# Performance work log

Measured on AMD Instinct MI355X. Metric: run time of the kernel, lower is better.

The kernel has to match this reference:

```python
import jax, jax.numpy as jnp
import numpy as np

N = 50000      # nodes
E = 1600000    # edges (avg degree 32)
D = 64         # d_node
DE = 32        # d_edge
H = 4          # heads
L = 3          # layers


def _ln(x, g, b):
    mu = x.mean(-1, keepdims=True)
    var = ((x - mu) ** 2).mean(-1, keepdims=True)
    return (x - mu) / jnp.sqrt(var + 1e-5) * g + b


def setup_inputs() -> dict:
    key = jax.random.key(0)
    ks = jax.random.split(key, 16)
    s = 0.05
    return {
        "node_features": jax.random.normal(ks[0], (N, D), jnp.float32),
        "edge_features": jax.random.normal(ks[1], (E, DE), jnp.float32),
        "edge_index": jax.random.randint(ks[2], (2, E), 0, N),
        "Wq": jax.random.normal(ks[3], (L, D, D), jnp.float32) * s,
        "Wk": jax.random.normal(ks[4], (L, D, D), jnp.float32) * s,
        "Wv": jax.random.normal(ks[5], (L, D, D), jnp.float32) * s,
        "Wo": jax.random.normal(ks[6], (L, D, D), jnp.float32) * s,
        "We": jax.random.normal(ks[7], (L, DE, H), jnp.float32) * s,   # edge-conditioned score bias
        "Wem": jax.random.normal(ks[8], (L, 2 * D + DE, DE), jnp.float32) * s,
        "bem": jnp.zeros((L, DE), jnp.float32),
        "gn": jnp.ones((L, D), jnp.float32),
        "bn": jnp.zeros((L, D), jnp.float32),
        "ge": jnp.ones((L, DE), jnp.float32),
        "be": jnp.zeros((L, DE), jnp.float32),
    }


def _delta_forward(h, e, src, dst, Wq, Wk, Wv, Wo, We, Wem, bem, gn, bn, ge, be):
    n = h.shape[0]
    dh = D // H
    for i in range(L):
        # --- node attention over edges (sparse, per-dst segment softmax) ---
        q = (h @ Wq[i]).reshape(n, H, dh)
        k = (h @ Wk[i]).reshape(n, H, dh)
        v = (h @ Wv[i]).reshape(n, H, dh)
        scores = jnp.einsum('ehd,ehd->eh', q[dst], k[src]) / jnp.sqrt(jnp.float32(dh))
        scores = scores + e @ We[i]                         # edge-conditioned bias [E,H]
        m = jax.ops.segment_max(scores, dst, num_segments=n)
        p = jnp.exp(scores - m[dst])
        denom = jax.ops.segment_sum(p, dst, num_segments=n)
        alpha = p / (denom[dst] + 1e-9)                      # [E,H]
        msg = (alpha[:, :, None] * v[src]).reshape(-1, D)    # [E,D]
        agg = jax.ops.segment_sum(msg, dst, num_segments=n)  # [N,D]
        h = _ln(h + agg @ Wo[i], gn[i], bn[i])
        # --- edge update conditioned on endpoint nodes ---
        emsg = jax.nn.gelu(jnp.concatenate([h[src], h[dst], e], axis=-1) @ Wem[i] + bem[i])
        e = _ln(e + emsg, ge[i], be[i])
    return h


def reference(node_features, edge_features, edge_index, Wq, Wk, Wv, Wo, We, Wem, bem, gn, bn, ge, be):
    src = edge_index[0]
    dst = edge_index[1]
    return _delta_forward(node_features, edge_features, src, dst,
                          Wq, Wk, Wv, Wo, We, Wem, bem, gn, bn, ge, be)
```

## Files before the change

### kernel.cpp

```cpp
#include <hip/hip_runtime.h>
#include <hip/hip_bf16.h>
#include <math.h>

#define NN 50000
#define NE 1600000
#define D 64
#define DE 32
#define H 4
#define DH 16
#define L 3

typedef __attribute__((ext_vector_type(8))) short bf16x8;
typedef __attribute__((ext_vector_type(8))) short s16x8;
typedef __attribute__((ext_vector_type(4))) float f32x4;

__device__ __forceinline__ short f2b(float f) {
    __hip_bfloat16 h = __float2bfloat16(f);
    short s;
    __builtin_memcpy(&s, &h, 2);
    return s;
}
__device__ __forceinline__ float b2f(unsigned short u) {
    unsigned int x = ((unsigned int)u) << 16;
    float f; __builtin_memcpy(&f, &x, 4); return f;
}
__device__ __forceinline__ float b2f_lo(unsigned int p) {
    unsigned int x = p << 16;
    float f; __builtin_memcpy(&f, &x, 4); return f;
}
__device__ __forceinline__ float b2f_hi(unsigned int p) {
    unsigned int x = p & 0xffff0000u;
    float f; __builtin_memcpy(&f, &x, 4); return f;
}


__global__ void deg_kernel(const int* __restrict__ dst, int* __restrict__ cnt) {
    int e = blockIdx.x * 256 + threadIdx.x;
    if (e >= NE) return;
    atomicAdd(&cnt[dst[e]], 1);
}

__global__ void block_sum_kernel(const int* __restrict__ cnt, int* __restrict__ bsum) {
    int b = blockIdx.x, t = threadIdx.x;
    int base = b * 1024 + t * 4;
    int s = 0;
#pragma unroll
    for (int i = 0; i < 4; i++) { int idx = base + i; if (idx < NN) s += cnt[idx]; }
#pragma unroll
    for (int off = 32; off; off >>= 1) s += __shfl_down(s, off);
    __shared__ int wsum[4];
    if ((t & 63) == 0) wsum[t >> 6] = s;
    __syncthreads();
    if (t == 0) bsum[b] = wsum[0] + wsum[1] + wsum[2] + wsum[3];
}

__global__ void scan_bsum_kernel(int* __restrict__ bsum, int nb) {
    if (blockIdx.x == 0 && threadIdx.x == 0) {
        int run = 0;
        for (int i = 0; i < nb; i++) { int c = bsum[i]; bsum[i] = run; run += c; }
    }
}

__global__ void scan_block_kernel(const int* __restrict__ cnt, const int* __restrict__ bsum,
                                  int* __restrict__ offsets) {
    int b = blockIdx.x, t = threadIdx.x;
    int base = b * 1024 + t * 4;
    int v[4]; int s = 0;
#pragma unroll
    for (int i = 0; i < 4; i++) { int idx = base + i; v[i] = (idx < NN) ? cnt[idx] : 0; s += v[i]; }
    int lane = t & 63, w = t >> 6;
    int x = s;
#pragma unroll
    for (int off = 1; off < 64; off <<= 1) {
        int y = __shfl_up(x, off);
        if (lane >= off) x += y;
    }
    __shared__ int wsum[4];
    if (lane == 63) wsum[w] = x;
    __syncthreads();
    int woff = 0;
    for (int i = 0; i < w; i++) woff += wsum[i];
    int run = bsum[b] + woff + x - s;
#pragma unroll
    for (int i = 0; i < 4; i++) {
        int idx = base + i;
        if (idx < NN) offsets[idx] = run;
        run += v[i];
    }
}

__global__ void scatter_kernel(const int* __restrict__ src, const int* __restrict__ dst,
                               const int* __restrict__ offsets,
                               int* __restrict__ cursor,
                               int* __restrict__ sorted_eid,
                               int* __restrict__ sorted_src,
                               int* __restrict__ sorted_dst) {
    int e = blockIdx.x * 256 + threadIdx.x;
    if (e >= NE) return;
    int d0 = dst[e];
    int pos = atomicAdd(&cursor[d0], 1);
    int position = offsets[d0] + pos;
    sorted_eid[position] = e;
    sorted_src[position] = src[e];
    sorted_dst[position] = d0;
}

__global__ void eperm_kernel(const float* __restrict__ e32, const int* __restrict__ sorted_eid,
                             const float* __restrict__ We0,
                             unsigned short* __restrict__ eb_s,
                             float* __restrict__ ebias_s) {
    int t = blockIdx.x * 256 + threadIdx.x;
    if (t >= NE * 4) return;
    int p = t >> 2;
    int c = (t & 3) * 8;
    int eid = sorted_eid[p];
    const float* ep = e32 + (size_t)eid * DE + c;
    float4 x0 = *(const float4*)(ep);
    float4 x1 = *(const float4*)(ep + 4);
    float e8[8] = {x0.x, x0.y, x0.z, x0.w, x1.x, x1.y, x1.z, x1.w};
    s16x8 ob;
#pragma unroll
    for (int i = 0; i < 8; i++) ob[i] = f2b(e8[i]);
    *(s16x8*)(eb_s + (size_t)p * DE + c) = ob;
    float p0 = 0.f, p1 = 0.f, p2 = 0.f, p3 = 0.f;
#pragma unroll
    for (int i = 0; i < 8; i++) {
        float4 w = *(const float4*)(We0 + (c + i) * 4);
        p0 += e8[i] * w.x; p1 += e8[i] * w.y; p2 += e8[i] * w.z; p3 += e8[i] * w.w;
    }
#pragma unroll
    for (int off = 1; off < 4; off <<= 1) {
        p0 += __shfl_xor(p0, off, 4);
        p1 += __shfl_xor(p1, off, 4);
        p2 += __shfl_xor(p2, off, 4);
        p3 += __shfl_xor(p3, off, 4);
    }
    if ((t & 3) == 0) {
        float4 o; o.x = p0; o.y = p1; o.z = p2; o.w = p3;
        *(float4*)(ebias_s + (size_t)p * H) = o;
    }
}

__global__ void wconv_kernel(const float* __restrict__ Wem, unsigned short* __restrict__ Wt) {
    int t = blockIdx.x * 256 + threadIdx.x;
    if (t >= L * 32 * 160) return;
    int l = t / 5120;
    int r = t % 5120;
    int n = r / 160;
    int k = r % 160;
    Wt[t] = (unsigned short)f2b(Wem[l * 5120 + k * 32 + n]);
}

__global__ void wsplit_kernel(const float* __restrict__ Wq, const float* __restrict__ Wk,
                              const float* __restrict__ Wv, const float* __restrict__ Wo,
                              unsigned short* __restrict__ WT_hi,
                              unsigned short* __restrict__ WT_lo) {
    int t = blockIdx.x * 256 + threadIdx.x;
    if (t >= L * 4 * 64 * 64) return;
    int k = t & 63;
    int n = (t >> 6) & 63;
    int mat = (t >> 12) & 3;
    int l = t >> 14;
    const float* W = (mat == 0) ? Wq : (mat == 1) ? Wk : (mat == 2) ? Wv : Wo;
    float w = W[l * 4096 + k * 64 + n];
    unsigned short hi = (unsigned short)f2b(w);
    float lo = w - b2f(hi);
    WT_hi[t] = hi;
    WT_lo[t] = (unsigned short)f2b(lo);
}

__global__ void hconv_kernel(const float* __restrict__ nf, float* __restrict__ h,
                             unsigned short* __restrict__ hb) {
    int t = blockIdx.x * 256 + threadIdx.x;
    if (t >= NN * D) return;
    float x = nf[t];
    h[t] = x;
    hb[t] = (unsigned short)f2b(x);
}


__global__ __launch_bounds__(256, 8)
void qkv_kernel(const float* __restrict__ h,
                const unsigned short* __restrict__ WT_hi,
                const unsigned short* __restrict__ WT_lo,
                float* __restrict__ q, unsigned int* __restrict__ kv) {
    int lane = threadIdx.x & 63;
    int wv = threadIdx.x >> 6;
    int m = lane & 15, quad = lane >> 4;
    int base = blockIdx.x * 16;

    const float* hp = h + (size_t)(base + m) * D + quad * 8;
    float af[16];
    *(f32x4*)&af[0]  = *(const f32x4*)(hp);
    *(f32x4*)&af[4]  = *(const f32x4*)(hp + 4);
    *(f32x4*)&af[8]  = *(const f32x4*)(hp + 32);
    *(f32x4*)&af[12] = *(const f32x4*)(hp + 36);
    bf16x8 a0h, a0l, a1h, a1l;
#pragma unroll
    for (int j = 0; j < 8; j++) {
        short h0 = f2b(af[j]);
        short h1 = f2b(af[8 + j]);
        a0h[j] = h0; a0l[j] = f2b(af[j] - b2f((unsigned short)h0));
        a1h[j] = h1; a1l[j] = f2b(af[8 + j] - b2f((unsigned short)h1));
    }

    f32x4 acc[3];
#pragma unroll
    for (int mat = 0; mat < 3; mat++) {
        const unsigned short* bh = WT_hi + ((size_t)mat * 64 + wv * 16 + m) * 64 + quad * 8;
        const unsigned short* bl = WT_lo + ((size_t)mat * 64 + wv * 16 + m) * 64 + quad * 8;
        bf16x8 bh0 = *(const bf16x8*)(bh);
        bf16x8 bh1 = *(const bf16x8*)(bh + 32);
        bf16x8 bl0 = *(const bf16x8*)(bl);
        bf16x8 bl1 = *(const bf16x8*)(bl + 32);
        f32x4 c = {0.f, 0.f, 0.f, 0.f};
        c = __builtin_amdgcn_mfma_f32_16x16x32_bf16(a0h, bh0, c, 0, 0, 0);
        c = __builtin_amdgcn_mfma_f32_16x16x32_bf16(a1h, bh1, c, 0, 0, 0);
        c = __builtin_amdgcn_mfma_f32_16x16x32_bf16(a0h, bl0, c, 0, 0, 0);
        c = __builtin_amdgcn_mfma_f32_16x16x32_bf16(a1h, bl1, c, 0, 0, 0);
        c = __builtin_amdgcn_mfma_f32_16x16x32_bf16(a0l, bh0, c, 0, 0, 0);
        c = __builtin_amdgcn_mfma_f32_16x16x32_bf16(a1l, bh1, c, 0, 0, 0);
        acc[mat] = c;
    }

#pragma unroll
    for (int reg = 0; reg < 4; reg++) {
        int row = base + quad * 4 + reg;
        int col = wv * 16 + m;
        q[(size_t)row * D + col] = acc[0][reg] * 0.25f;
        unsigned int kb = (unsigned short)f2b(acc[1][reg]);
        unsigned int vb = (unsigned short)f2b(acc[2][reg]);
        kv[(size_t)row * D + col] = (vb << 16) | kb;
    }
}

__global__ void attn_kernel(const float* __restrict__ q, const unsigned int* __restrict__ kv,
                            const float* __restrict__ ebias_s,
                            const int* __restrict__ sorted_src,
                            const int* __restrict__ offsets,
                            float* __restrict__ agg) {
    int node = blockIdx.x * 4 + threadIdx.y;
    node = __builtin_amdgcn_readfirstlane(node);
    if (node >= NN) return;
    int lane = threadIdx.x;
    int hh = lane >> 4;
    float qv = q[node * D + lane];
    int beg = offsets[node];
    int end = (node == NN - 1) ? NE : offsets[node + 1];
    float mmax = -INFINITY, den = 0.f, acc = 0.f;
    int i = beg;
    for (; i + 8 <= end; i += 8) {
        int ss[8]; unsigned int kk8[8]; float bb8[8], dd[8];
#pragma unroll
        for (int u = 0; u < 8; u++) ss[u] = sorted_src[i + u];
#pragma unroll
        for (int u = 0; u < 8; u++) kk8[u] = kv[ss[u] * D + lane];
#pragma unroll
        for (int u = 0; u < 8; u++) bb8[u] = ebias_s[(i + u) * H + hh];
#pragma unroll
        for (int u = 0; u < 8; u++) dd[u] = qv * b2f_lo(kk8[u]);
#pragma unroll
        for (int off = 1; off < 16; off <<= 1) {
#pragma unroll
            for (int u = 0; u < 8; u++) dd[u] += __shfl_xor(dd[u], off, 16);
        }
        float nm = mmax;
#pragma unroll
        for (int u = 0; u < 8; u++) { dd[u] += bb8[u]; nm = fmaxf(nm, dd[u]); }
        float scale = __expf(mmax - nm);
        float ps = 0.f, av = 0.f;
#pragma unroll
        for (int u = 0; u < 8; u++) {
            float p = __expf(dd[u] - nm);
            ps += p;
            av += p * b2f_hi(kk8[u]);
        }
        den = den * scale + ps;
        acc = acc * scale + av;
        mmax = nm;
    }
    for (; i < end; i++) {
        int s = sorted_src[i];
        unsigned int kvv = kv[s * D + lane];
        float b = ebias_s[i * H + hh];
        float dot = qv * b2f_lo(kvv);
#pragma unroll
        for (int off = 1; off < 16; off <<= 1) dot += __shfl_xor(dot, off, 16);
        float score = dot + b;
        float nm = fmaxf(mmax, score);
        float scale = __expf(mmax - nm);
        float p = __expf(score - nm);
        den = den * scale + p;
        acc = acc * scale + p * b2f_hi(kvv);
        mmax = nm;
    }
    agg[node * D + lane] = acc / (den + 1e-9f);
}

__global__ __launch_bounds__(256, 8)
void node_update_kernel(float* __restrict__ h, const float* __restrict__ agg,
                        const unsigned short* __restrict__ WoT_hi,
                        const unsigned short* __restrict__ WoT_lo,
                        const float* __restrict__ gn,
                        const float* __restrict__ bn,
                        unsigned short* __restrict__ hb) {
    __shared__ float sx[16][68];
    int lane = threadIdx.x & 63;
    int wv = threadIdx.x >> 6;
    int m = lane & 15, quad = lane >> 4;
    int base = blockIdx.x * 16;

    const float* ap = agg + (size_t)(base + m) * D + quad * 8;
    float af[16];
    *(f32x4*)&af[0]  = *(const f32x4*)(ap);
    *(f32x4*)&af[4]  = *(const f32x4*)(ap + 4);
    *(f32x4*)&af[8]  = *(const f32x4*)(ap + 32);
    *(f32x4*)&af[12] = *(const f32x4*)(ap + 36);
    bf16x8 a0h, a0l, a1h, a1l;
#pragma unroll
    for (int j = 0; j < 8; j++) {
        short h0 = f2b(af[j]);
        short h1 = f2b(af[8 + j]);
        a0h[j] = h0; a0l[j] = f2b(af[j] - b2f((unsigned short)h0));
        a1h[j] = h1; a1l[j] = f2b(af[8 + j] - b2f((unsigned short)h1));
    }
    const unsigned short* bh = WoT_hi + ((size_t)wv * 16 + m) * 64 + quad * 8;
    const unsigned short* bl = WoT_lo + ((size_t)wv * 16 + m) * 64 + quad * 8;
    bf16x8 bh0 = *(const bf16x8*)(bh);
    bf16x8 bh1 = *(const bf16x8*)(bh + 32);
    bf16x8 bl0 = *(const bf16x8*)(bl);
    bf16x8 bl1 = *(const bf16x8*)(bl + 32);
    f32x4 c = {0.f, 0.f, 0.f, 0.f};
    c = __builtin_amdgcn_mfma_f32_16x16x32_bf16(a0h, bh0, c, 0, 0, 0);
    c = __builtin_amdgcn_mfma_f32_16x16x32_bf16(a1h, bh1, c, 0, 0, 0);
    c = __builtin_amdgcn_mfma_f32_16x16x32_bf16(a0h, bl0, c, 0, 0, 0);
    c = __builtin_amdgcn_mfma_f32_16x16x32_bf16(a1h, bl1, c, 0, 0, 0);
    c = __builtin_amdgcn_mfma_f32_16x16x32_bf16(a0l, bh0, c, 0, 0, 0);
    c = __builtin_amdgcn_mfma_f32_16x16x32_bf16(a1l, bh1, c, 0, 0, 0);

#pragma unroll
    for (int reg = 0; reg < 4; reg++) {
        int row = quad * 4 + reg;
        int col = wv * 16 + m;
        sx[row][col] = c[reg] + h[(size_t)(base + row) * D + col];
    }
    __syncthreads();

    float gcol = gn[lane], bcol = bn[lane];
#pragma unroll
    for (int it = 0; it < 4; it++) {
        int ln = wv * 4 + it;
        int node = base + ln;
        float x = sx[ln][lane];
        float sum = x, sq = x * x;
#pragma unroll
        for (int off = 32; off; off >>= 1) {
            sum += __shfl_xor(sum, off);
            sq += __shfl_xor(sq, off);
        }
        float mu = sum * (1.f / 64.f);
        float var = sq * (1.f / 64.f) - mu * mu;
        float out = (x - mu) * rsqrtf(var + 1e-5f) * gcol + bcol;
        h[(size_t)node * D + lane] = out;
        hb[(size_t)node * D + lane] = (unsigned short)f2b(out);
    }
}

__global__ __launch_bounds__(256, 4)
void edge_update_mfma_kernel(const unsigned short* __restrict__ hb,
                             unsigned short* __restrict__ eb_s,
                             const int* __restrict__ sorted_src,
                             const int* __restrict__ sorted_dst,
                             const unsigned short* __restrict__ Wt,
                             const float* __restrict__ bem,
                             const float* __restrict__ ge,
                             const float* __restrict__ be,
                             const float* __restrict__ We_next,
                             float* __restrict__ ebias_s,
                             int do_bias, int do_estore) {
    __shared__ __align__(16) unsigned short sWt[32][168];
    __shared__ __align__(16) float ytr[4][16][36];
    int tid = threadIdx.x;
    int wave = tid >> 6;
    int lane = tid & 63;
    int we = blockIdx.x * 64 + wave * 16;
    int m = lane & 15;
    int quad = lane >> 4;
    int p_m = we + m;
    int s_idx = sorted_src[p_m], d_idx = sorted_dst[p_m];

    const unsigned short* as = hb + (size_t)s_idx * D + quad * 8;
    const unsigned short* ad = hb + (size_t)d_idx * D + quad * 8;
    bf16x8 a_s0 = *(const bf16x8*)(as);
    bf16x8 a_s1 = *(const bf16x8*)(as + 32);
    bf16x8 a_d0 = *(const bf16x8*)(ad);
    bf16x8 a_d1 = *(const bf16x8*)(ad + 32);
    bf16x8 ea = *(const bf16x8*)(eb_s + (size_t)p_m * DE + quad * 8);

    {
        const unsigned int* Wt32 = (const unsigned int*)Wt;
#pragma unroll
        for (int it = 0; it < 10; it++) {
            int i = tid + it * 256;
            int sh = i * 2;
            int r = sh / 160, c = sh % 160;
            *(unsigned int*)&sWt[r][c] = Wt32[i];
        }
    }

    bf16x8 wb;
#pragma unroll
    for (int j = 0; j < 8; j++) {
        float w = (do_bias && m < 4) ? We_next[(quad * 8 + j) * 4 + m] : 0.f;
        wb[j] = f2b(w);
    }

    __syncthreads();

    f32x4 c0 = {0.f, 0.f, 0.f, 0.f};
    f32x4 c1 = {0.f, 0.f, 0.f, 0.f};
    const unsigned short* w0 = &sWt[m][quad * 8];
    const unsigned short* w1 = &sWt[m + 16][quad * 8];

#pragma unroll
    for (int ks = 0; ks < 4; ks++) {
        bf16x8 a = (ks == 0) ? a_s0 : (ks == 1) ? a_s1 : (ks == 2) ? a_d0 : a_d1;
        bf16x8 b0 = *(const bf16x8*)(w0 + ks * 32);
        bf16x8 b1 = *(const bf16x8*)(w1 + ks * 32);
        c0 = __builtin_amdgcn_mfma_f32_16x16x32_bf16(a, b0, c0, 0, 0, 0);
        c1 = __builtin_amdgcn_mfma_f32_16x16x32_bf16(a, b1, c1, 0, 0, 0);
    }
    {
        bf16x8 b0 = *(const bf16x8*)(w0 + 4 * 32);
        bf16x8 b1 = *(const bf16x8*)(w1 + 4 * 32);
        c0 = __builtin_amdgcn_mfma_f32_16x16x32_bf16(ea, b0, c0, 0, 0, 0);
        c1 = __builtin_amdgcn_mfma_f32_16x16x32_bf16(ea, b1, c1, 0, 0, 0);
    }

    float bm0 = bem[m], bm1 = bem[m + 16];
#pragma unroll
    for (int reg = 0; reg < 4; reg++) {
        int row = quad * 4 + reg;
        float y0 = c0[reg] + bm0;
        float y1 = c1[reg] + bm1;
        float u0 = 1.5957691216057308f * (y0 + 0.044715f * y0 * y0 * y0);
        float u1 = 1.5957691216057308f * (y1 + 0.044715f * y1 * y1 * y1);
        float t0 = 1.f - 2.f / (1.f + __expf(u0));
        float t1 = 1.f - 2.f / (1.f + __expf(u1));
        ytr[wave][row][m] = 0.5f * y0 * (1.f + t0);
        ytr[wave][row][m + 16] = 0.5f * y1 * (1.f + t1);
    }
    __syncthreads();

    float y[8];
    *(f32x4*)&y[0] = *(const f32x4*)&ytr[wave][m][quad * 8];
    *(f32x4*)&y[4] = *(const f32x4*)&ytr[wave][m][quad * 8 + 4];
    float s = 0.f, sq = 0.f;
#pragma unroll
    for (int j = 0; j < 8; j++) {
        y[j] += b2f((unsigned short)ea[j]);
        s += y[j];
        sq += y[j] * y[j];
    }
    s += __shfl_xor(s, 16); s += __shfl_xor(s, 32);
    sq += __shfl_xor(sq, 16); sq += __shfl_xor(sq, 32);
    float mu = s * (1.f / 32.f);
    float var = sq * (1.f / 32.f) - mu * mu;
    float inv = rsqrtf(var + 1e-5f);

    float4 g0 = *(const float4*)(ge + quad * 8);
    float4 g1 = *(const float4*)(ge + quad * 8 + 4);
    float4 b0 = *(const float4*)(be + quad * 8);
    float4 b1 = *(const float4*)(be + quad * 8 + 4);
    float gg[8] = {g0.x, g0.y, g0.z, g0.w, g1.x, g1.y, g1.z, g1.w};
    float bbv[8] = {b0.x, b0.y, b0.z, b0.w, b1.x, b1.y, b1.z, b1.w};
    bf16x8 zb;
#pragma unroll
    for (int j = 0; j < 8; j++) {
        float z = (y[j] - mu) * inv * gg[j] + bbv[j];
        zb[j] = f2b(z);
    }
    if (do_estore) {
        *(s16x8*)(eb_s + (size_t)p_m * DE + quad * 8) = zb;
    }
    if (do_bias) {
        f32x4 db = {0.f, 0.f, 0.f, 0.f};
        db = __builtin_amdgcn_mfma_f32_16x16x32_bf16(zb, wb, db, 0, 0, 0);
        if (m < 4) {
#pragma unroll
            for (int reg = 0; reg < 4; reg++) {
                ebias_s[(we + quad * 4 + reg) * H + m] = db[reg];
            }
        }
    }
}

extern "C" void kernel_launch(void* const* d_in, const int* in_sizes, int n_in,
                              void* d_out, int out_size, void* d_ws, size_t ws_size,
                              hipStream_t stream) {
    const float* node_features = (const float*)d_in[0];
    const float* e = (const float*)d_in[1];
    const int* edge_index = (const int*)d_in[2];
    const int* src = edge_index;
    const int* dst = edge_index + NE;
    const float* Wq = (const float*)d_in[3];
    const float* Wk = (const float*)d_in[4];
    const float* Wv = (const float*)d_in[5];
    const float* Wo = (const float*)d_in[6];
    const float* We = (const float*)d_in[7];
    const float* Wem = (const float*)d_in[8];
    const float* bem = (const float*)d_in[9];
    const float* gn = (const float*)d_in[10];
    const float* bn = (const float*)d_in[11];
    const float* ge = (const float*)d_in[12];
    const float* be = (const float*)d_in[13];

    float* h = (float*)d_out;

    float* ws = (float*)d_ws;
    float* q = ws;
    unsigned int* kv = (unsigned int*)(q + NN * D);
    float* agg = (float*)(kv + NN * D);
    float* ebias_s = agg + NN * D;
    int* offsets = (int*)(ebias_s + (size_t)NE * H);
    int* cursor = offsets + NN;
    int* bsum = cursor + NN;
    int* sorted_eid = bsum + 64;
    int* sorted_src = sorted_eid + NE;
    int* sorted_dst = sorted_src + NE;
    unsigned short* Wt = (unsigned short*)(sorted_dst + NE);
    unsigned short* hb = Wt + L * 32 * 160;
    unsigned short* eb_s = hb + NN * D;
    unsigned short* WT_hi = eb_s + (size_t)NE * DE;
    unsigned short* WT_lo = WT_hi + L * 4 * 64 * 64;

    const int NB = (NN + 1023) / 1024;

    hipMemsetAsync(cursor, 0, NN * sizeof(int), stream);
    deg_kernel<<<(NE + 255) / 256, 256, 0, stream>>>(dst, cursor);
    block_sum_kernel<<<NB, 256, 0, stream>>>(cursor, bsum);
    scan_bsum_kernel<<<1, 64, 0, stream>>>(bsum, NB);
    scan_block_kernel<<<NB, 256, 0, stream>>>(cursor, bsum, offsets);
    hipMemsetAsync(cursor, 0, NN * sizeof(int), stream);
    scatter_kernel<<<(NE + 255) / 256, 256, 0, stream>>>(src, dst, offsets, cursor,
                                                         sorted_eid, sorted_src, sorted_dst);
    eperm_kernel<<<(NE * 4 + 255) / 256, 256, 0, stream>>>(e, sorted_eid, We, eb_s, ebias_s);
    wconv_kernel<<<(L * 32 * 160 + 255) / 256, 256, 0, stream>>>(Wem, Wt);
    wsplit_kernel<<<(L * 4 * 64 * 64 + 255) / 256, 256, 0, stream>>>(Wq, Wk, Wv, Wo,
                                                                     WT_hi, WT_lo);
    hconv_kernel<<<(NN * D + 255) / 256, 256, 0, stream>>>(node_features, h, hb);

    for (int layer = 0; layer < L; layer++) {
        const unsigned short* WT_hi_l = WT_hi + (size_t)layer * 4 * 4096;
        const unsigned short* WT_lo_l = WT_lo + (size_t)layer * 4 * 4096;
        const unsigned short* Wt_l = Wt + layer * 32 * 160;
        const float* bem_l = bem + layer * DE;
        const float* gn_l = gn + layer * D;
        const float* bn_l = bn + layer * D;
        const float* ge_l = ge + layer * DE;
        const float* be_l = be + layer * DE;

        qkv_kernel<<<NN / 16, 256, 0, stream>>>(h, WT_hi_l, WT_lo_l, q, kv);
        attn_kernel<<<NN / 4, dim3(64, 4), 0, stream>>>(q, kv, ebias_s, sorted_src,
                                                        offsets, agg);
        node_update_kernel<<<NN / 16, 256, 0, stream>>>(h, agg,
                                                        WT_hi_l + 3 * 4096,
                                                        WT_lo_l + 3 * 4096,
                                                        gn_l, bn_l, hb);
        if (layer < L - 1) {
            const float* We_next = We + (layer + 1) * DE * H;
            edge_update_mfma_kernel<<<NE / 64, 256, 0, stream>>>(hb, eb_s, sorted_src,
                                                                 sorted_dst, Wt_l,
                                                                 bem_l, ge_l, be_l,
                                                                 We_next, ebias_s,
                                                                 1, layer == 0 ? 1 : 0);
        }
    }
}
```

Before: 1.132 ms.

## Keep edge-update weights in registers and process four edge tiles per wave

The edge-update kernel no longer stages the 32x160 weight matrix in shared memory for every 64-edge block. Each wave now loads its weight fragments into registers once and loops over four 16-edge tiles, so there are four times fewer blocks and the block-wide barrier and shared-memory weight copy are gone. The sorted src/dst gather moves from the atomic scatter kernel into the coalesced eperm pass, and the single-thread serial block-sum scan becomes a wave shuffle scan. The cost is more registers per thread, which may lower occupancy, and less latency hiding within each wave because the gathers for each tile are done serially.

```diff
diff --git a/kernel.cpp b/kernel.cpp
--- a/kernel.cpp
+++ b/kernel.cpp
@@ -55,10 +55,15 @@
 }
 
 __global__ void scan_bsum_kernel(int* __restrict__ bsum, int nb) {
-    if (blockIdx.x == 0 && threadIdx.x == 0) {
-        int run = 0;
-        for (int i = 0; i < nb; i++) { int c = bsum[i]; bsum[i] = run; run += c; }
-    }
+    int t = threadIdx.x;
+    int v = (t < nb) ? bsum[t] : 0;
+    int x = v;
+#pragma unroll
+    for (int off = 1; off < 64; off <<= 1) {
+        int y = __shfl_up(x, off);
+        if (t >= off) x += y;
+    }
+    if (t < nb) bsum[t] = x - v;
 }
 
 __global__ void scan_block_kernel(const int* __restrict__ cnt, const int* __restrict__ bsum,
@@ -89,26 +94,24 @@
     }
 }
 
-__global__ void scatter_kernel(const int* __restrict__ src, const int* __restrict__ dst,
+__global__ void scatter_kernel(const int* __restrict__ dst,
                                const int* __restrict__ offsets,
                                int* __restrict__ cursor,
-                               int* __restrict__ sorted_eid,
-                               int* __restrict__ sorted_src,
-                               int* __restrict__ sorted_dst) {
+                               int* __restrict__ sorted_eid) {
     int e = blockIdx.x * 256 + threadIdx.x;
     if (e >= NE) return;
     int d0 = dst[e];
     int pos = atomicAdd(&cursor[d0], 1);
-    int position = offsets[d0] + pos;
-    sorted_eid[position] = e;
-    sorted_src[position] = src[e];
-    sorted_dst[position] = d0;
+    sorted_eid[offsets[d0] + pos] = e;
 }
 
 __global__ void eperm_kernel(const float* __restrict__ e32, const int* __restrict__ sorted_eid,
+                             const int* __restrict__ src, const int* __restrict__ dst,
                              const float* __restrict__ We0,
                              unsigned short* __restrict__ eb_s,
-                             float* __restrict__ ebias_s) {
+                             float* __restrict__ ebias_s,
+                             int* __restrict__ sorted_src,
+                             int* __restrict__ sorted_dst) {
     int t = blockIdx.x * 256 + threadIdx.x;
     if (t >= NE * 4) return;
     int p = t >> 2;
@@ -138,6 +141,8 @@
     if ((t & 3) == 0) {
         float4 o; o.x = p0; o.y = p1; o.z = p2; o.w = p3;
         *(float4*)(ebias_s + (size_t)p * H) = o;
+        sorted_src[p] = src[eid];
+        sorted_dst[p] = dst[eid];
     }
 }
 
@@ -378,118 +383,105 @@
                              const float* __restrict__ We_next,
                              float* __restrict__ ebias_s,
                              int do_bias, int do_estore) {
-    __shared__ __align__(16) unsigned short sWt[32][168];
     __shared__ __align__(16) float ytr[4][16][36];
     int tid = threadIdx.x;
     int wave = tid >> 6;
     int lane = tid & 63;
-    int we = blockIdx.x * 64 + wave * 16;
+    int wbase = blockIdx.x * 256 + wave * 64;
     int m = lane & 15;
     int quad = lane >> 4;
-    int p_m = we + m;
-    int s_idx = sorted_src[p_m], d_idx = sorted_dst[p_m];
-
-    const unsigned short* as = hb + (size_t)s_idx * D + quad * 8;
-    const unsigned short* ad = hb + (size_t)d_idx * D + quad * 8;
-    bf16x8 a_s0 = *(const bf16x8*)(as);
-    bf16x8 a_s1 = *(const bf16x8*)(as + 32);
-    bf16x8 a_d0 = *(const bf16x8*)(ad);
-    bf16x8 a_d1 = *(const bf16x8*)(ad + 32);
-    bf16x8 ea = *(const bf16x8*)(eb_s + (size_t)p_m * DE + quad * 8);
-
-    {
-        const unsigned int* Wt32 = (const unsigned int*)Wt;
-#pragma unroll
-        for (int it = 0; it < 10; it++) {
-            int i = tid + it * 256;
-            int sh = i * 2;
-            int r = sh / 160, c = sh % 160;
-            *(unsigned int*)&sWt[r][c] = Wt32[i];
-        }
-    }
-
+
+    const unsigned short* w0 = Wt + m * 160 + quad * 8;
+    const unsigned short* w1 = Wt + (m + 16) * 160 + quad * 8;
+    bf16x8 B0[5], B1[5];
+#pragma unroll
+    for (int ks = 0; ks < 5; ks++) {
+        B0[ks] = *(const bf16x8*)(w0 + ks * 32);
+        B1[ks] = *(const bf16x8*)(w1 + ks * 32);
+    }
     bf16x8 wb;
 #pragma unroll
     for (int j = 0; j < 8; j++) {
         float w = (do_bias && m < 4) ? We_next[(quad * 8 + j) * 4 + m] : 0.f;
         wb[j] = f2b(w);
     }
-
-    __syncthreads();
-
-    f32x4 c0 = {0.f, 0.f, 0.f, 0.f};
-    f32x4 c1 = {0.f, 0.f, 0.f, 0.f};
-    const unsigned short* w0 = &sWt[m][quad * 8];
-    const unsigned short* w1 = &sWt[m + 16][quad * 8];
-
-#pragma unroll
-    for (int ks = 0; ks < 4; ks++) {
-        bf16x8 a = (ks == 0) ? a_s0 : (ks == 1) ? a_s1 : (ks == 2) ? a_d0 : a_d1;
-        bf16x8 b0 = *(const bf16x8*)(w0 + ks * 32);
-        bf16x8 b1 = *(const bf16x8*)(w1 + ks * 32);
-        c0 = __builtin_amdgcn_mfma_f32_16x16x32_bf16(a, b0, c0, 0, 0, 0);
-        c1 = __builtin_amdgcn_mfma_f32_16x16x32_bf16(a, b1, c1, 0, 0, 0);
-    }
-    {
-        bf16x8 b0 = *(const bf16x8*)(w0 + 4 * 32);
-        bf16x8 b1 = *(const bf16x8*)(w1 + 4 * 32);
-        c0 = __builtin_amdgcn_mfma_f32_16x16x32_bf16(ea, b0, c0, 0, 0, 0);
-        c1 = __builtin_amdgcn_mfma_f32_16x16x32_bf16(ea, b1, c1, 0, 0, 0);
-    }
-
     float bm0 = bem[m], bm1 = bem[m + 16];
-#pragma unroll
-    for (int reg = 0; reg < 4; reg++) {
-        int row = quad * 4 + reg;
-        float y0 = c0[reg] + bm0;
-        float y1 = c1[reg] + bm1;
-        float u0 = 1.5957691216057308f * (y0 + 0.044715f * y0 * y0 * y0);
-        float u1 = 1.5957691216057308f * (y1 + 0.044715f * y1 * y1 * y1);
-        float t0 = 1.f - 2.f / (1.f + __expf(u0));
-        float t1 = 1.f - 2.f / (1.f + __expf(u1));
-        ytr[wave][row][m] = 0.5f * y0 * (1.f + t0);
-        ytr[wave][row][m + 16] = 0.5f * y1 * (1.f + t1);
-    }
-    __syncthreads();
-
-    float y[8];
-    *(f32x4*)&y[0] = *(const f32x4*)&ytr[wave][m][quad * 8];
-    *(f32x4*)&y[4] = *(const f32x4*)&ytr[wave][m][quad * 8 + 4];
-    float s = 0.f, sq = 0.f;
-#pragma unroll
-    for (int j = 0; j < 8; j++) {
-        y[j] += b2f((unsigned short)ea[j]);
-        s += y[j];
-        sq += y[j] * y[j];
-    }
-    s += __shfl_xor(s, 16); s += __shfl_xor(s, 32);
-    sq += __shfl_xor(sq, 16); sq += __shfl_xor(sq, 32);
-    float mu = s * (1.f / 32.f);
-    float var = sq * (1.f / 32.f) - mu * mu;
-    float inv = rsqrtf(var + 1e-5f);
-
-    float4 g0 = *(const float4*)(ge + quad * 8);
-    float4 g1 = *(const float4*)(ge + quad * 8 + 4);
-    float4 b0 = *(const float4*)(be + quad * 8);
-    float4 b1 = *(const float4*)(be + quad * 8 + 4);
-    float gg[8] = {g0.x, g0.y, g0.z, g0.w, g1.x, g1.y, g1.z, g1.w};
-    float bbv[8] = {b0.x, b0.y, b0.z, b0.w, b1.x, b1.y, b1.z, b1.w};
-    bf16x8 zb;
-#pragma unroll
-    for (int j = 0; j < 8; j++) {
-        float z = (y[j] - mu) * inv * gg[j] + bbv[j];
-        zb[j] = f2b(z);
-    }
-    if (do_estore) {
-        *(s16x8*)(eb_s + (size_t)p_m * DE + quad * 8) = zb;
-    }
-    if (do_bias) {
-        f32x4 db = {0.f, 0.f, 0.f, 0.f};
-        db = __builtin_amdgcn_mfma_f32_16x16x32_bf16(zb, wb, db, 0, 0, 0);
-        if (m < 4) {
-#pragma unroll
-            for (int reg = 0; reg < 4; reg++) {
-                ebias_s[(we + quad * 4 + reg) * H + m] = db[reg];
+    float4 g0v = *(const float4*)(ge + quad * 8);
+    float4 g1v = *(const float4*)(ge + quad * 8 + 4);
+    float4 b0v = *(const float4*)(be + quad * 8);
+    float4 b1v = *(const float4*)(be + quad * 8 + 4);
+    float gg[8] = {g0v.x, g0v.y, g0v.z, g0v.w, g1v.x, g1v.y, g1v.z, g1v.w};
+    float bbv[8] = {b0v.x, b0v.y, b0v.z, b0v.w, b1v.x, b1v.y, b1v.z, b1v.w};
+
+    for (int g = 0; g < 4; g++) {
+        int we = wbase + g * 16;
+        int p_m = we + m;
+        int s_idx = sorted_src[p_m], d_idx = sorted_dst[p_m];
+        const unsigned short* as = hb + (size_t)s_idx * D + quad * 8;
+        const unsigned short* ad = hb + (size_t)d_idx * D + quad * 8;
+        bf16x8 a_s0 = *(const bf16x8*)(as);
+        bf16x8 a_s1 = *(const bf16x8*)(as + 32);
+        bf16x8 a_d0 = *(const bf16x8*)(ad);
+        bf16x8 a_d1 = *(const bf16x8*)(ad + 32);
+        bf16x8 ea = *(const bf16x8*)(eb_s + (size_t)p_m * DE + quad * 8);
+
+        f32x4 c0 = {0.f, 0.f, 0.f, 0.f};
+        f32x4 c1 = {0.f, 0.f, 0.f, 0.f};
+#pragma unroll
+        for (int ks = 0; ks < 4; ks++) {
+            bf16x8 a = (ks == 0) ? a_s0 : (ks == 1) ? a_s1 : (ks == 2) ? a_d0 : a_d1;
+            c0 = __builtin_amdgcn_mfma_f32_16x16x32_bf16(a, B0[ks], c0, 0, 0, 0);
+            c1 = __builtin_amdgcn_mfma_f32_16x16x32_bf16(a, B1[ks], c1, 0, 0, 0);
+        }
+        c0 = __builtin_amdgcn_mfma_f32_16x16x32_bf16(ea, B0[4], c0, 0, 0, 0);
+        c1 = __builtin_amdgcn_mfma_f32_16x16x32_bf16(ea, B1[4], c1, 0, 0, 0);
+
+#pragma unroll
+        for (int reg = 0; reg < 4; reg++) {
+            int row = quad * 4 + reg;
+            float y0 = c0[reg] + bm0;
+            float y1 = c1[reg] + bm1;
+            float u0 = 1.5957691216057308f * (y0 + 0.044715f * y0 * y0 * y0);
+            float u1 = 1.5957691216057308f * (y1 + 0.044715f * y1 * y1 * y1);
+            float t0 = 1.f - 2.f / (1.f + __expf(u0));
+            float t1 = 1.f - 2.f / (1.f + __expf(u1));
+            ytr[wave][row][m] = 0.5f * y0 * (1.f + t0);
+            ytr[wave][row][m + 16] = 0.5f * y1 * (1.f + t1);
+        }
+
+        float y[8];
+        *(f32x4*)&y[0] = *(const f32x4*)&ytr[wave][m][quad * 8];
+        *(f32x4*)&y[4] = *(const f32x4*)&ytr[wave][m][quad * 8 + 4];
+        float s = 0.f, sq = 0.f;
+#pragma unroll
+        for (int j = 0; j < 8; j++) {
+            y[j] += b2f((unsigned short)ea[j]);
+            s += y[j];
+            sq += y[j] * y[j];
+        }
+        s += __shfl_xor(s, 16); s += __shfl_xor(s, 32);
+        sq += __shfl_xor(sq, 16); sq += __shfl_xor(sq, 32);
+        float mu = s * (1.f / 32.f);
+        float var = sq * (1.f / 32.f) - mu * mu;
+        float inv = rsqrtf(var + 1e-5f);
+
+        bf16x8 zb;
+#pragma unroll
+        for (int j = 0; j < 8; j++) {
+            float z = (y[j] - mu) * inv * gg[j] + bbv[j];
+            zb[j] = f2b(z);
+        }
+        if (do_estore) {
+            *(s16x8*)(eb_s + (size_t)p_m * DE + quad * 8) = zb;
+        }
+        if (do_bias) {
+            f32x4 db = {0.f, 0.f, 0.f, 0.f};
+            db = __builtin_amdgcn_mfma_f32_16x16x32_bf16(zb, wb, db, 0, 0, 0);
+            if (m < 4) {
+#pragma unroll
+                for (int reg = 0; reg < 4; reg++) {
+                    ebias_s[(we + quad * 4 + reg) * H + m] = db[reg];
+                }
             }
         }
     }
@@ -542,9 +534,10 @@
     scan_bsum_kernel<<<1, 64, 0, stream>>>(bsum, NB);
     scan_block_kernel<<<NB, 256, 0, stream>>>(cursor, bsum, offsets);
     hipMemsetAsync(cursor, 0, NN * sizeof(int), stream);
-    scatter_kernel<<<(NE + 255) / 256, 256, 0, stream>>>(src, dst, offsets, cursor,
-                                                         sorted_eid, sorted_src, sorted_dst);
-    eperm_kernel<<<(NE * 4 + 255) / 256, 256, 0, stream>>>(e, sorted_eid, We, eb_s, ebias_s);
+    scatter_kernel<<<(NE + 255) / 256, 256, 0, stream>>>(dst, offsets, cursor, sorted_eid);
+    eperm_kernel<<<(NE * 4 + 255) / 256, 256, 0, stream>>>(e, sorted_eid, src, dst, We,
+                                                           eb_s, ebias_s,
+                                                           sorted_src, sorted_dst);
     wconv_kernel<<<(L * 32 * 160 + 255) / 256, 256, 0, stream>>>(Wem, Wt);
     wsplit_kernel<<<(L * 4 * 64 * 64 + 255) / 256, 256, 0, stream>>>(Wq, Wk, Wv, Wo,
                                                                      WT_hi, WT_lo);
@@ -569,11 +562,11 @@
                                                         gn_l, bn_l, hb);
         if (layer < L - 1) {
             const float* We_next = We + (layer + 1) * DE * H;
-            edge_update_mfma_kernel<<<NE / 64, 256, 0, stream>>>(hb, eb_s, sorted_src,
-                                                                 sorted_dst, Wt_l,
-                                                                 bem_l, ge_l, be_l,
-                                                                 We_next, ebias_s,
-                                                                 1, layer == 0 ? 1 : 0);
-        }
-    }
-}
+            edge_update_mfma_kernel<<<NE / 256, 256, 0, stream>>>(hb, eb_s, sorted_src,
+                                                                  sorted_dst, Wt_l,
+                                                                  bem_l, ge_l, be_l,
+                                                                  We_next, ebias_s,
+                                                                  1, layer == 0 ? 1 : 0);
+        }
+    }
+}
```

Result: no change. 1.135 ms (+0.3%).
